# Kernel optimization log

Measured on AMD Instinct MI355X. Metric: run time of the kernel, lower is better.

The kernel has to match this reference:

```python
import jax, jax.numpy as jnp
import numpy as np
from jax import lax

NEG = jnp.float32(-1e30)  # log-domain 'zero'
BLANK = 0


def setup_inputs() -> dict:
    T, N, C, S = 512, 512, 80, 128
    k0, k1, k2, k3 = jax.random.split(jax.random.key(0), 4)
    logits = jax.random.normal(k0, (T, N, C), dtype=jnp.float32)
    log_probs = jax.nn.log_softmax(logits, axis=-1)  # CTCLoss expects log-probs
    targets = jax.random.randint(k1, (N, S), 1, C).astype(jnp.int32)  # labels in [1, C-1], blank=0 excluded
    input_lengths = jax.random.randint(k2, (N,), T // 2, T + 1).astype(jnp.int32)
    target_lengths = jax.random.randint(k3, (N,), S // 2, S + 1).astype(jnp.int32)
    return {"log_probs": log_probs, "targets": targets,
            "input_lengths": input_lengths, "target_lengths": target_lengths}


def _ctc_loss(log_probs, targets, input_lengths, target_lengths):
    # log_probs: (T, N, C) log-probabilities; targets: (N, S) labels (no blanks)
    T, N, C = log_probs.shape
    S = targets.shape[1]
    L = 2 * S + 1  # extended label length: blank-interleaved

    # extended targets: [blank, y1, blank, y2, ..., yS, blank]  -> (N, L)
    ext = jnp.zeros((N, L), jnp.int32).at[:, 1::2].set(targets)
    # skip transition (s-2 -> s) allowed only if ext[s] != ext[s-2]
    # (blank positions have ext[s]==ext[s-2]==blank, so this also forbids blank skips)
    skip_ok = jnp.pad(ext[:, 2:] != ext[:, :-2], ((0, 0), (2, 0)), constant_values=False)

    # emission log-probs on the lattice: (T, N, L)
    emit = jnp.take_along_axis(log_probs, jnp.broadcast_to(ext[None], (T, N, L)), axis=2)

    # alpha at t=0: only lattice positions 0 (blank) and 1 (first label) reachable
    alpha0 = jnp.full((N, L), NEG).at[:, 0].set(emit[0, :, 0]).at[:, 1].set(emit[0, :, 1])

    def step(alpha, xs):
        em, t = xs  # em: (N, L)
        a1 = jnp.pad(alpha[:, :-1], ((0, 0), (1, 0)), constant_values=NEG)
        a2 = jnp.where(skip_ok,
                       jnp.pad(alpha[:, :-2], ((0, 0), (2, 0)), constant_values=NEG), NEG)
        m = jnp.maximum(alpha, jnp.maximum(a1, a2))
        lse = m + jnp.log(jnp.exp(alpha - m) + jnp.exp(a1 - m) + jnp.exp(a2 - m))
        new = lse + em
        # freeze alpha for finished sequences (t >= input_length)
        alpha_new = jnp.where((t < input_lengths)[:, None], new, alpha)
        return alpha_new, None

    alpha_T, _ = lax.scan(step, alpha0, (emit[1:], jnp.arange(1, T, dtype=jnp.int32)))

    # final states: last blank (2*tl) and last label (2*tl - 1)
    i1 = (2 * target_lengths)[:, None]
    v1 = jnp.take_along_axis(alpha_T, i1, axis=1)[:, 0]
    v2 = jnp.take_along_axis(alpha_T, i1 - 1, axis=1)[:, 0]
    m = jnp.maximum(v1, v2)
    loss = -(m + jnp.log(jnp.exp(v1 - m) + jnp.exp(v2 - m)))
    # zero_infinity=True: infeasible alignments -> 0 loss
    loss = jnp.where(jnp.isfinite(loss) & (loss < 1e10), loss, 0.0)
    return loss  # (N,) reduction='none'


def reference(log_probs, targets, input_lengths, target_lengths):
    return _ctc_loss(log_probs, targets, input_lengths, target_lengths)
```

## Files before the change

### kernel.cpp

```cpp
#include <hip/hip_runtime.h>


#define NEGC  (-1.0e30f)
#define LOG2E 1.4426950408889634f
#define LN2   0.6931471805599453f

constexpr int T_ = 512;
constexpr int C_ = 80;
constexpr int S_ = 128;
constexpr int U_ = 8;
constexpr int WROW = 520;

__device__ __forceinline__ float exp2a(float x) { return __builtin_amdgcn_exp2f(x); }
__device__ __forceinline__ float log2a(float x) { return __builtin_amdgcn_logf(x); }

template <int CTRL>
__device__ __forceinline__ float dppf(float old_, float src) {
    return __int_as_float(__builtin_amdgcn_update_dpp(
        __float_as_int(old_), __float_as_int(src), CTRL, 0xF, 0xF, false));
}

__device__ __forceinline__ float lse2(float x, float y) {
    float m = fmaxf(x, y);
    return m + log2a(1.0f + exp2a(-fabsf(x - y)));
}
__device__ __forceinline__ float lse3(float x, float y, float z) {
    float m = fmaxf(x, fmaxf(y, z));
    return m + log2a(exp2a(x - m) + exp2a(y - m) + exp2a(z - m));
}

__global__ __launch_bounds__(64) void ctc_half(
    const float* __restrict__ lp, const int* __restrict__ tgt,
    const int* __restrict__ ilen, const int* __restrict__ tlen,
    float* __restrict__ ws, int N)
{
    const int b   = blockIdx.x;
    const int n   = b >> 1;
    const int dir = b & 1;
    const int l   = threadIdx.x;

    float* ga = ws + (size_t)n * WROW;
    float* gg = ga + 260;

    const int* tn = tgt + n * S_;
    const int ext1 = tn[2 * l];
    const int ext3 = tn[2 * l + 1];
    const int prev = (l > 0) ? tn[2 * l - 1] : 0;
    const bool skip1 = (l > 0) && (ext1 != prev);
    const bool skip3 = (ext3 != ext1);
    const bool skb3  = (l < 63) && (tn[2 * l + 2] != ext3);

    int len = ilen[n];
    len = len < 1 ? 1 : (len > T_ ? T_ : len);
    const int mid = len >> 1;

    const size_t rstride = (size_t)N * C_;
    const float* lpn = lp + (size_t)n * C_;
    const float* pB = lpn;
    const float* p1 = lpn + ext1;
    const float* p3 = lpn + ext3;

    float rb[U_], r1[U_], r3[U_];

    if (dir == 0) {
        const int last = mid - 1 > 0 ? mid - 1 : 0;
        #pragma unroll
        for (int u = 0; u < U_; ++u) {
            const int r = u + 1;
            const int rc = r < mid ? r : last;
            const size_t o = (size_t)rc * rstride;
            rb[r & 7] = pB[o]; r1[r & 7] = p1[o]; r3[r & 7] = p3[o];
        }
        float a0 = NEGC, a1 = NEGC, a2 = NEGC, a3 = NEGC, a4 = NEGC;
        {
            const float i0 = pB[0] * LOG2E;
            const float i1 = p1[0] * LOG2E;
            if (l == 0) { a0 = i0; a1 = i1; }
        }
        for (int tb = 1; tb < mid; tb += U_) {
            #pragma unroll
            for (int u = 0; u < U_; ++u) {
                const int t = tb + u;
                const int slot = (1 + u) & 7;
                const float eb = rb[slot] * LOG2E;
                const float e1 = r1[slot] * LOG2E;
                const float e3 = r3[slot] * LOG2E;
                const int rr = t + U_;
                const int rc = rr < mid ? rr : last;
                const size_t o = (size_t)rc * rstride;
                const float nrb = pB[o], nr1 = p1[o], nr3 = p3[o];
                if (t < mid) {
                    const float sm1 = dppf<0x138>(NEGC, a3);
                    const float M = fmaxf(fmaxf(fmaxf(a0, a1), fmaxf(a2, a3)),
                                          fmaxf(a4, sm1));
                    const float q0 = exp2a(a0 - M);
                    const float q1 = exp2a(a1 - M);
                    const float q2 = exp2a(a2 - M);
                    const float q3 = exp2a(a3 - M);
                    const float q4 = exp2a(a4 - M);
                    const float qs = exp2a(sm1 - M);
                    const float Mb = M + eb;
                    a0 = log2a(q0 + qs)                      + Mb;
                    a1 = log2a(q1 + q0 + (skip1 ? qs : 0.f)) + M + e1;
                    a2 = log2a(q2 + q1)                      + Mb;
                    a3 = log2a(q3 + q2 + (skip3 ? q1 : 0.f)) + M + e3;
                    a4 = log2a(q4 + q3)                      + Mb;
                }
                rb[slot] = nrb; r1[slot] = nr1; r3[slot] = nr3;
            }
        }
        ga[4 * l + 0] = a0; ga[4 * l + 1] = a1;
        ga[4 * l + 2] = a2; ga[4 * l + 3] = a3;
        if (l == 63) ga[256] = a4;
    } else {
        const int fe = len - 1;
        #pragma unroll
        for (int u = 0; u < U_; ++u) {
            int rc = fe - 1 - u; if (rc < 0) rc = 0;
            const size_t o = (size_t)rc * rstride;
            rb[u] = pB[o]; r1[u] = p1[o]; r3[u] = p3[o];
        }
        const int tl = tlen[n];
        const int sA = 2 * tl, sB = 2 * tl - 1;
        float g0, g1, g2, g3, g4;
        {
            const size_t o = (size_t)fe * rstride;
            const float ebi = pB[o] * LOG2E;
            const float e1i = p1[o] * LOG2E;
            const float e3i = p3[o] * LOG2E;
            const int s0 = 4 * l;
            g0 = (s0     == sA)                 ? ebi : NEGC;
            g1 = (s0 + 1 == sA || s0 + 1 == sB) ? e1i : NEGC;
            g2 = (s0 + 2 == sA)                 ? ebi : NEGC;
            g3 = (s0 + 3 == sA || s0 + 3 == sB) ? e3i : NEGC;
            g4 = (l == 63 && 256 == sA)         ? ebi : NEGC;
        }
        for (int tb = fe - 1; tb >= mid; tb -= U_) {
            #pragma unroll
            for (int u = 0; u < U_; ++u) {
                const int t = tb - u;
                const int slot = ((fe - 1 - tb) + u) & 7;
                const float eb = rb[slot] * LOG2E;
                const float e1 = r1[slot] * LOG2E;
                const float e3 = r3[slot] * LOG2E;
                int rc = t - U_; if (rc < 0) rc = 0;
                const size_t o = (size_t)rc * rstride;
                const float nrb = pB[o], nr1 = p1[o], nr3 = p3[o];
                if (t >= mid) {
                    const float nx0 = dppf<0x130>(g4,   g0);
                    const float nx1 = dppf<0x130>(NEGC, g1);
                    const float M = fmaxf(fmaxf(fmaxf(g0, g1), fmaxf(g2, g3)),
                                          fmaxf(nx0, nx1));
                    const float q0 = exp2a(g0 - M);
                    const float q1 = exp2a(g1 - M);
                    const float q2 = exp2a(g2 - M);
                    const float q3 = exp2a(g3 - M);
                    const float qx0 = exp2a(nx0 - M);
                    const float qx1 = exp2a(nx1 - M);
                    const float skb1q = (ext3 != ext1) ? q3 : 0.f;
                    g0 = log2a(q0 + q1)                        + M + eb;
                    g1 = log2a(q1 + q2 + skb1q)                + M + e1;
                    g2 = log2a(q2 + q3)                        + M + eb;
                    g3 = log2a(q3 + qx0 + (skb3 ? qx1 : 0.f))  + M + e3;
                    g4 = g4 + eb;
                }
                rb[slot] = nrb; r1[slot] = nr1; r3[slot] = nr3;
            }
        }
        gg[4 * l + 0] = g0; gg[4 * l + 1] = g1;
        gg[4 * l + 2] = g2; gg[4 * l + 3] = g3;
        if (l == 63) gg[256] = g4;
    }
}

__global__ __launch_bounds__(64) void ctc_comb(
    const float* __restrict__ ws, const int* __restrict__ tgt,
    const int* __restrict__ ilen, const int* __restrict__ tlen,
    float* __restrict__ out, int N)
{
    const int n = blockIdx.x;
    const int l = threadIdx.x;
    const float* ga = ws + (size_t)n * WROW;
    const float* gg = ga + 260;

    int len = ilen[n];
    len = len < 1 ? 1 : (len > T_ ? T_ : len);
    const int tl = tlen[n];

    if (len == 1) {
        if (l == 0) {
            const float v1 = ga[2 * tl];
            const float v2 = (2 * tl >= 1) ? ga[2 * tl - 1] : NEGC;
            float loss = -lse2(v1, v2) * LN2;
            if (!(loss < 1e10f) || !isfinite(loss)) loss = 0.0f;
            out[n] = loss;
        }
        return;
    }

    const int* tn = tgt + n * S_;
    const int ext1 = tn[2 * l];
    const int ext3 = tn[2 * l + 1];
    const int prev = (l > 0) ? tn[2 * l - 1] : 0;
    const bool skip1 = (l > 0) && (ext1 != prev);
    const bool skip3 = (ext3 != ext1);

    const int s0 = 4 * l;
    const float Am1 = (l > 0) ? ga[s0 - 1] : NEGC;
    const float A0 = ga[s0], A1 = ga[s0 + 1], A2 = ga[s0 + 2], A3 = ga[s0 + 3];
    const float v0 = lse2(A0, Am1)                    + gg[s0];
    const float v1 = lse3(A1, A0, skip1 ? Am1 : NEGC) + gg[s0 + 1];
    const float v2 = lse2(A2, A1)                     + gg[s0 + 2];
    const float v3 = lse3(A3, A2, skip3 ? A1 : NEGC)  + gg[s0 + 3];
    const float v4 = (l == 63) ? (lse2(ga[256], A3) + gg[256]) : NEGC;

    float m = fmaxf(fmaxf(v0, v1), fmaxf(fmaxf(v2, v3), v4));
    float ssum = exp2a(v0 - m) + exp2a(v1 - m) + exp2a(v2 - m)
               + exp2a(v3 - m) + exp2a(v4 - m);
    float M = m;
    #pragma unroll
    for (int d = 1; d < 64; d <<= 1) M = fmaxf(M, __shfl_xor(M, d));
    float r = ssum * exp2a(m - M);
    #pragma unroll
    for (int d = 1; d < 64; d <<= 1) r += __shfl_xor(r, d);
    if (l == 0) {
        float loss = -LN2 * (M + log2a(r));
        if (!(loss < 1e10f) || !isfinite(loss)) loss = 0.0f;
        out[n] = loss;
    }
}

__global__ __launch_bounds__(128) void ctc_fused(
    const float* __restrict__ lp, const int* __restrict__ tgt,
    const int* __restrict__ ilen, const int* __restrict__ tlen,
    float* __restrict__ out, int N)
{
    const int n    = blockIdx.x;
    const int wave = threadIdx.x >> 6;
    const int l    = threadIdx.x & 63;

    __shared__ float ga[2 * S_ + 1];
    __shared__ float gg[2 * S_ + 1];

    const int* tn = tgt + n * S_;
    const int ext1 = tn[2 * l];
    const int ext3 = tn[2 * l + 1];
    const int prev = (l > 0) ? tn[2 * l - 1] : 0;
    const bool skip1 = (l > 0) && (ext1 != prev);
    const bool skip3 = (ext3 != ext1);
    const bool skb1 = (tn[2 * l + 1] != tn[2 * l]);
    const bool skb3 = (l < 63) && (tn[2 * l + 2] != tn[2 * l + 1]);

    int len = ilen[n];
    len = len < 1 ? 1 : (len > T_ ? T_ : len);
    const int mid = len >> 1;

    const size_t rstride = (size_t)N * C_;
    const float* lpn = lp + (size_t)n * C_;
    const float* pB = lpn;
    const float* p1 = lpn + ext1;
    const float* p3 = lpn + ext3;

    float rb[U_], r1[U_], r3[U_];

    if (wave == 0) {
        const int last = mid - 1 > 0 ? mid - 1 : 0;
        #pragma unroll
        for (int u = 0; u < U_; ++u) {
            const int r = u + 1;
            const int rc = r < mid ? r : last;
            const size_t o = (size_t)rc * rstride;
            rb[r & 7] = pB[o]; r1[r & 7] = p1[o]; r3[r & 7] = p3[o];
        }
        float a0 = NEGC, a1 = NEGC, a2 = NEGC, a3 = NEGC, a4 = NEGC;
        {
            const float i0 = pB[0] * LOG2E;
            const float i1 = p1[0] * LOG2E;
            if (l == 0) { a0 = i0; a1 = i1; }
        }
        for (int tb = 1; tb < mid; tb += U_) {
            #pragma unroll
            for (int u = 0; u < U_; ++u) {
                const int t = tb + u;
                const int slot = (1 + u) & 7;
                const float eb = rb[slot] * LOG2E;
                const float e1 = r1[slot] * LOG2E;
                const float e3 = r3[slot] * LOG2E;
                const int rr = t + U_;
                const int rc = rr < mid ? rr : last;
                const size_t o = (size_t)rc * rstride;
                const float nrb = pB[o], nr1 = p1[o], nr3 = p3[o];
                if (t < mid) {
                    const float sm1 = dppf<0x138>(NEGC, a3);
                    const float z1 = skip1 ? sm1 : NEGC;
                    const float z3 = skip3 ? a1  : NEGC;
                    const float n0 = lse2(a0, sm1)    + eb;
                    const float n1 = lse3(a1, a0, z1) + e1;
                    const float n2 = lse2(a2, a1)     + eb;
                    const float n3 = lse3(a3, a2, z3) + e3;
                    const float n4 = lse2(a4, a3)     + eb;
                    a0 = n0; a1 = n1; a2 = n2; a3 = n3; a4 = n4;
                }
                rb[slot] = nrb; r1[slot] = nr1; r3[slot] = nr3;
            }
        }
        ga[4 * l + 0] = a0; ga[4 * l + 1] = a1;
        ga[4 * l + 2] = a2; ga[4 * l + 3] = a3;
        if (l == 63) ga[256] = a4;
    } else {
        const int fe = len - 1;
        #pragma unroll
        for (int u = 0; u < U_; ++u) {
            int rc = fe - 1 - u; if (rc < 0) rc = 0;
            const size_t o = (size_t)rc * rstride;
            rb[u] = pB[o]; r1[u] = p1[o]; r3[u] = p3[o];
        }
        const int tl = tlen[n];
        const int sA = 2 * tl, sB = 2 * tl - 1;
        float g0, g1, g2, g3, g4;
        {
            const size_t o = (size_t)fe * rstride;
            const float ebi = pB[o] * LOG2E;
            const float e1i = p1[o] * LOG2E;
            const float e3i = p3[o] * LOG2E;
            const int s0 = 4 * l;
            g0 = (s0     == sA)                 ? ebi : NEGC;
            g1 = (s0 + 1 == sA || s0 + 1 == sB) ? e1i : NEGC;
            g2 = (s0 + 2 == sA)                 ? ebi : NEGC;
            g3 = (s0 + 3 == sA || s0 + 3 == sB) ? e3i : NEGC;
            g4 = (l == 63 && 256 == sA)         ? ebi : NEGC;
        }
        for (int tb = fe - 1; tb >= mid; tb -= U_) {
            #pragma unroll
            for (int u = 0; u < U_; ++u) {
                const int t = tb - u;
                const int slot = ((fe - 1 - tb) + u) & 7;
                const float eb = rb[slot] * LOG2E;
                const float e1 = r1[slot] * LOG2E;
                const float e3 = r3[slot] * LOG2E;
                int rc = t - U_; if (rc < 0) rc = 0;
                const size_t o = (size_t)rc * rstride;
                const float nrb = pB[o], nr1 = p1[o], nr3 = p3[o];
                if (t >= mid) {
                    const float nx0 = dppf<0x130>(g4,   g0);
                    const float nx1 = dppf<0x130>(NEGC, g1);
                    const float z1 = skb1 ? g3  : NEGC;
                    const float z3 = skb3 ? nx1 : NEGC;
                    const float n0 = lse2(g0, g1)      + eb;
                    const float n1 = lse3(g1, g2, z1)  + e1;
                    const float n2 = lse2(g2, g3)      + eb;
                    const float n3 = lse3(g3, nx0, z3) + e3;
                    const float n4 = g4 + eb;
                    g0 = n0; g1 = n1; g2 = n2; g3 = n3; g4 = n4;
                }
                rb[slot] = nrb; r1[slot] = nr1; r3[slot] = nr3;
            }
        }
        gg[4 * l + 0] = g0; gg[4 * l + 1] = g1;
        gg[4 * l + 2] = g2; gg[4 * l + 3] = g3;
        if (l == 63) gg[256] = g4;
    }

    __syncthreads();

    if (wave == 0) {
        const int tl = tlen[n];
        if (len == 1) {
            if (l == 0) {
                const float v1 = ga[2 * tl];
                const float v2 = (2 * tl >= 1) ? ga[2 * tl - 1] : NEGC;
                float loss = -lse2(v1, v2) * LN2;
                if (!(loss < 1e10f) || !isfinite(loss)) loss = 0.0f;
                out[n] = loss;
            }
            return;
        }
        const int s0 = 4 * l;
        const float Am1 = (l > 0) ? ga[s0 - 1] : NEGC;
        const float A0 = ga[s0], A1 = ga[s0 + 1], A2 = ga[s0 + 2], A3 = ga[s0 + 3];
        const float v0 = lse2(A0, Am1)                    + gg[s0];
        const float v1 = lse3(A1, A0, skip1 ? Am1 : NEGC) + gg[s0 + 1];
        const float v2 = lse2(A2, A1)                     + gg[s0 + 2];
        const float v3 = lse3(A3, A2, skip3 ? A1 : NEGC)  + gg[s0 + 3];
        const float v4 = (l == 63) ? (lse2(ga[256], A3) + gg[256]) : NEGC;

        float m = fmaxf(fmaxf(v0, v1), fmaxf(fmaxf(v2, v3), v4));
        float ssum = exp2a(v0 - m) + exp2a(v1 - m) + exp2a(v2 - m)
                   + exp2a(v3 - m) + exp2a(v4 - m);
        float M = m;
        #pragma unroll
        for (int d = 1; d < 64; d <<= 1) M = fmaxf(M, __shfl_xor(M, d));
        float r = ssum * exp2a(m - M);
        #pragma unroll
        for (int d = 1; d < 64; d <<= 1) r += __shfl_xor(r, d);
        if (l == 0) {
            float loss = -LN2 * (M + log2a(r));
            if (!(loss < 1e10f) || !isfinite(loss)) loss = 0.0f;
            out[n] = loss;
        }
    }
}

extern "C" void kernel_launch(void* const* d_in, const int* in_sizes, int n_in,
                              void* d_out, int out_size, void* d_ws, size_t ws_size,
                              hipStream_t stream) {
    const float* lp  = (const float*)d_in[0];
    const int*   tg  = (const int*)  d_in[1];
    const int*   il  = (const int*)  d_in[2];
    const int*   tl  = (const int*)  d_in[3];
    float*       out = (float*)d_out;
    const int N = in_sizes[2];
    const size_t need = (size_t)N * WROW * sizeof(float);
    if (ws_size >= need) {
        ctc_half<<<2 * N, 64, 0, stream>>>(lp, tg, il, tl, (float*)d_ws, N);
        ctc_comb<<<N, 64, 0, stream>>>((const float*)d_ws, tg, il, tl, out, N);
    } else {
        ctc_fused<<<N, 128, 0, stream>>>(lp, tg, il, tl, out, N);
    }
}
```

Before: 156.6 us.

## Switch CTC alpha/beta recursion from log domain to scaled linear domain

Replaces the per-step log-sum-exp (six exp2 and five log2 transcendentals per lane per step) with linear-domain probabilities. Each lane keeps an integer exponent, and values are renormalised using exponent-bit extraction and power-of-two scaling. Neighbour exponents are exchanged with DPP so values can be aligned across lanes, and dead lanes inherit their neighbour's exponent. Only three exp2 calls are left per step, for the emissions. The cost is extra integer and ALU work per step and some risk of underflow or precision differences from the capped alignment shift.

```diff
diff --git a/kernel.cpp b/kernel.cpp
--- a/kernel.cpp
+++ b/kernel.cpp
@@ -10,6 +10,8 @@
 constexpr int S_ = 128;
 constexpr int U_ = 8;
 constexpr int WROW = 520;
+constexpr int BIGE = 1 << 24;
+constexpr int DCAP = 110;
 
 __device__ __forceinline__ float exp2a(float x) { return __builtin_amdgcn_exp2f(x); }
 __device__ __forceinline__ float log2a(float x) { return __builtin_amdgcn_logf(x); }
@@ -18,6 +20,15 @@
 __device__ __forceinline__ float dppf(float old_, float src) {
     return __int_as_float(__builtin_amdgcn_update_dpp(
         __float_as_int(old_), __float_as_int(src), CTRL, 0xF, 0xF, false));
+}
+template <int CTRL>
+__device__ __forceinline__ int dppi(int old_, int src) {
+    return __builtin_amdgcn_update_dpp(old_, src, CTRL, 0xF, 0xF, false);
+}
+
+__device__ __forceinline__ float pow2f(int k) {
+    int kc = k < -127 ? -127 : k;
+    return __int_as_float((kc + 127) << 23);
 }
 
 __device__ __forceinline__ float lse2(float x, float y) {
@@ -71,47 +82,63 @@
             const size_t o = (size_t)rc * rstride;
             rb[r & 7] = pB[o]; r1[r & 7] = p1[o]; r3[r & 7] = p3[o];
         }
-        float a0 = NEGC, a1 = NEGC, a2 = NEGC, a3 = NEGC, a4 = NEGC;
+        float m0 = 0.f, m1 = 0.f, m2 = 0.f, m3 = 0.f, m4 = 0.f;
+        int E = 0;
         {
-            const float i0 = pB[0] * LOG2E;
-            const float i1 = p1[0] * LOG2E;
-            if (l == 0) { a0 = i0; a1 = i1; }
+            const float i0 = exp2a(pB[0] * LOG2E);
+            const float i1 = exp2a(p1[0] * LOG2E);
+            if (l == 0) { m0 = i0; m1 = i1; }
         }
         for (int tb = 1; tb < mid; tb += U_) {
             #pragma unroll
             for (int u = 0; u < U_; ++u) {
                 const int t = tb + u;
                 const int slot = (1 + u) & 7;
-                const float eb = rb[slot] * LOG2E;
-                const float e1 = r1[slot] * LOG2E;
-                const float e3 = r3[slot] * LOG2E;
+                const float pb  = exp2a(rb[slot] * LOG2E);
+                const float pe1 = exp2a(r1[slot] * LOG2E);
+                const float pe3 = exp2a(r3[slot] * LOG2E);
                 const int rr = t + U_;
                 const int rc = rr < mid ? rr : last;
                 const size_t o = (size_t)rc * rstride;
                 const float nrb = pB[o], nr1 = p1[o], nr3 = p3[o];
                 if (t < mid) {
-                    const float sm1 = dppf<0x138>(NEGC, a3);
-                    const float M = fmaxf(fmaxf(fmaxf(a0, a1), fmaxf(a2, a3)),
-                                          fmaxf(a4, sm1));
-                    const float q0 = exp2a(a0 - M);
-                    const float q1 = exp2a(a1 - M);
-                    const float q2 = exp2a(a2 - M);
-                    const float q3 = exp2a(a3 - M);
-                    const float q4 = exp2a(a4 - M);
-                    const float qs = exp2a(sm1 - M);
-                    const float Mb = M + eb;
-                    a0 = log2a(q0 + qs)                      + Mb;
-                    a1 = log2a(q1 + q0 + (skip1 ? qs : 0.f)) + M + e1;
-                    a2 = log2a(q2 + q1)                      + Mb;
-                    a3 = log2a(q3 + q2 + (skip3 ? q1 : 0.f)) + M + e3;
-                    a4 = log2a(q4 + q3)                      + Mb;
+                    const float s3  = dppf<0x138>(0.f, m3);
+                    const int   Eup = dppi<0x138>(E, E);
+                    const int   dE  = Eup - E;
+                    const int   dc  = dE > DCAP ? DCAP : dE;
+                    const float fsc = pow2f(dc - dE);
+                    const float aln = s3 * pow2f(dc);
+
+                    const float m0f = m0 * fsc, m1f = m1 * fsc, m2f = m2 * fsc;
+                    const float m3f = m3 * fsc, m4f = m4 * fsc;
+                    const float z1 = skip1 ? aln : 0.f;
+                    const float z3 = skip3 ? m1f : 0.f;
+                    const float n0 = (m0f + aln)       * pb;
+                    const float n1 = (m1f + m0f + z1)  * pe1;
+                    const float n2 = (m2f + m1f)       * pb;
+                    const float n3 = (m3f + m2f + z3)  * pe3;
+                    const float n4 = (m4f + m3f)       * pb;
+
+                    const float mx = fmaxf(fmaxf(n0, n1), fmaxf(fmaxf(n2, n3), n4));
+                    const bool dead = (mx == 0.0f);
+                    const int  eb = (__float_as_int(mx) >> 23) & 0xFF;
+                    const float sc = __int_as_float((254 - eb) << 23);
+                    m0 = n0 * sc; m1 = n1 * sc; m2 = n2 * sc;
+                    m3 = n3 * sc; m4 = n4 * sc;
+                    const int Eb = Eup - dc;
+                    const int E1 = dead ? E : (Eb + eb - 127);
+                    const int Ein = dppi<0x138>(E1, E1);
+                    E = dead ? Ein : E1;
                 }
                 rb[slot] = nrb; r1[slot] = nr1; r3[slot] = nr3;
             }
         }
-        ga[4 * l + 0] = a0; ga[4 * l + 1] = a1;
-        ga[4 * l + 2] = a2; ga[4 * l + 3] = a3;
-        if (l == 63) ga[256] = a4;
+        const float Ef = (float)E;
+        ga[4 * l + 0] = fmaxf(log2a(m0) + Ef, NEGC);
+        ga[4 * l + 1] = fmaxf(log2a(m1) + Ef, NEGC);
+        ga[4 * l + 2] = fmaxf(log2a(m2) + Ef, NEGC);
+        ga[4 * l + 3] = fmaxf(log2a(m3) + Ef, NEGC);
+        if (l == 63) ga[256] = fmaxf(log2a(m4) + Ef, NEGC);
     } else {
         const int fe = len - 1;
         #pragma unroll
@@ -123,53 +150,70 @@
         const int tl = tlen[n];
         const int sA = 2 * tl, sB = 2 * tl - 1;
         float g0, g1, g2, g3, g4;
+        int E = (4 * l > sA) ? -BIGE : 0;
         {
             const size_t o = (size_t)fe * rstride;
-            const float ebi = pB[o] * LOG2E;
-            const float e1i = p1[o] * LOG2E;
-            const float e3i = p3[o] * LOG2E;
+            const float ebv = exp2a(pB[o] * LOG2E);
+            const float e1v = exp2a(p1[o] * LOG2E);
+            const float e3v = exp2a(p3[o] * LOG2E);
             const int s0 = 4 * l;
-            g0 = (s0     == sA)                 ? ebi : NEGC;
-            g1 = (s0 + 1 == sA || s0 + 1 == sB) ? e1i : NEGC;
-            g2 = (s0 + 2 == sA)                 ? ebi : NEGC;
-            g3 = (s0 + 3 == sA || s0 + 3 == sB) ? e3i : NEGC;
-            g4 = (l == 63 && 256 == sA)         ? ebi : NEGC;
+            g0 = (s0     == sA)                 ? ebv : 0.f;
+            g1 = (s0 + 1 == sA || s0 + 1 == sB) ? e1v : 0.f;
+            g2 = (s0 + 2 == sA)                 ? ebv : 0.f;
+            g3 = (s0 + 3 == sA || s0 + 3 == sB) ? e3v : 0.f;
+            g4 = (l == 63 && 256 == sA)         ? ebv : 0.f;
         }
         for (int tb = fe - 1; tb >= mid; tb -= U_) {
             #pragma unroll
             for (int u = 0; u < U_; ++u) {
                 const int t = tb - u;
                 const int slot = ((fe - 1 - tb) + u) & 7;
-                const float eb = rb[slot] * LOG2E;
-                const float e1 = r1[slot] * LOG2E;
-                const float e3 = r3[slot] * LOG2E;
+                const float pb  = exp2a(rb[slot] * LOG2E);
+                const float pe1 = exp2a(r1[slot] * LOG2E);
+                const float pe3 = exp2a(r3[slot] * LOG2E);
                 int rc = t - U_; if (rc < 0) rc = 0;
                 const size_t o = (size_t)rc * rstride;
                 const float nrb = pB[o], nr1 = p1[o], nr3 = p3[o];
                 if (t >= mid) {
-                    const float nx0 = dppf<0x130>(g4,   g0);
-                    const float nx1 = dppf<0x130>(NEGC, g1);
-                    const float M = fmaxf(fmaxf(fmaxf(g0, g1), fmaxf(g2, g3)),
-                                          fmaxf(nx0, nx1));
-                    const float q0 = exp2a(g0 - M);
-                    const float q1 = exp2a(g1 - M);
-                    const float q2 = exp2a(g2 - M);
-                    const float q3 = exp2a(g3 - M);
-                    const float qx0 = exp2a(nx0 - M);
-                    const float qx1 = exp2a(nx1 - M);
-                    const float skb1q = (ext3 != ext1) ? q3 : 0.f;
-                    g0 = log2a(q0 + q1)                        + M + eb;
-                    g1 = log2a(q1 + q2 + skb1q)                + M + e1;
-                    g2 = log2a(q2 + q3)                        + M + eb;
-                    g3 = log2a(q3 + qx0 + (skb3 ? qx1 : 0.f))  + M + e3;
-                    g4 = g4 + eb;
+                    const float x0  = dppf<0x130>(g4,  g0);
+                    const float x1  = dppf<0x130>(0.f, g1);
+                    const int   Eup = dppi<0x130>(E, E);
+                    const int   dE  = Eup - E;
+                    const int   dc  = dE > DCAP ? DCAP : dE;
+                    const float fsc = pow2f(dc - dE);
+                    const float al  = pow2f(dc);
+                    const float nx0 = x0 * al, nx1 = x1 * al;
+
+                    const float g0f = g0 * fsc, g1f = g1 * fsc, g2f = g2 * fsc;
+                    const float g3f = g3 * fsc, g4f = g4 * fsc;
+                    const float z1 = skip3 ? g3f : 0.f;
+                    const float z3 = skb3  ? nx1 : 0.f;
+                    const float n0 = (g0f + g1f)        * pb;
+                    const float n1 = (g1f + g2f + z1)   * pe1;
+                    const float n2 = (g2f + g3f)        * pb;
+                    const float n3 = (g3f + nx0 + z3)   * pe3;
+                    const float n4 = g4f                * pb;
+
+                    const float mx = fmaxf(fmaxf(n0, n1), fmaxf(fmaxf(n2, n3), n4));
+                    const bool dead = (mx == 0.0f);
+                    const int  eb = (__float_as_int(mx) >> 23) & 0xFF;
+                    const float sc = __int_as_float((254 - eb) << 23);
+                    g0 = n0 * sc; g1 = n1 * sc; g2 = n2 * sc;
+                    g3 = n3 * sc; g4 = n4 * sc;
+                    const int Eb = Eup - dc;
+                    const int E1 = dead ? E : (Eb + eb - 127);
+                    const int Ein = dppi<0x130>(E1, E1);
+                    E = dead ? Ein : E1;
                 }
                 rb[slot] = nrb; r1[slot] = nr1; r3[slot] = nr3;
             }
         }
-        gg[4 * l + 0] = g0; gg[4 * l + 1] = g1;
-        gg[4 * l + 2] = g2; gg[4 * l + 3] = g3;
-        if (l == 63) gg[256] = g4;
+        const float Ef = (float)E;
+        gg[4 * l + 0] = fmaxf(log2a(g0) + Ef, NEGC);
+        gg[4 * l + 1] = fmaxf(log2a(g1) + Ef, NEGC);
+        gg[4 * l + 2] = fmaxf(log2a(g2) + Ef, NEGC);
+        gg[4 * l + 3] = fmaxf(log2a(g3) + Ef, NEGC);
+        if (l == 63) gg[256] = fmaxf(log2a(g4) + Ef, NEGC);
     }
 }
 
```

Measured after the change: 161.6 us. 3.2% more time.

## Stage per-sequence log-prob rows into LDS as fp16 before recurrence

Applied to the files above, without the earlier changes.

Each block bulk-loads its half of the time rows for sequence n with coalesced float4 reads, converts them to fp16 and stores them in a 40KB shared table. The recurrence then gathers emissions from LDS with a one-step software prefetch, replacing the 8-deep register ring of scattered global loads. The aim is to take global gather latency off the serial time loop. In exchange, fp16 rounding of the log-probs adds precision loss, and the large LDS allocation may reduce occupancy. No barrier is used because each block is a single wave.

```diff
diff --git a/kernel.cpp b/kernel.cpp
--- a/kernel.cpp
+++ b/kernel.cpp
@@ -1,4 +1,5 @@
 #include <hip/hip_runtime.h>
+#include <hip/hip_fp16.h>
 
 
 #define NEGC  (-1.0e30f)
@@ -11,6 +12,8 @@
 constexpr int U_ = 8;
 constexpr int WROW = 520;
 
+#define WAIT_LGKM0 __builtin_amdgcn_s_waitcnt(0xC07F)
+
 __device__ __forceinline__ float exp2a(float x) { return __builtin_amdgcn_exp2f(x); }
 __device__ __forceinline__ float log2a(float x) { return __builtin_amdgcn_logf(x); }
 
@@ -18,6 +21,13 @@
 __device__ __forceinline__ float dppf(float old_, float src) {
     return __int_as_float(__builtin_amdgcn_update_dpp(
         __float_as_int(old_), __float_as_int(src), CTRL, 0xF, 0xF, false));
+}
+
+__device__ __forceinline__ unsigned short f2h(float x) {
+    return __half_as_ushort(__float2half(x));
+}
+__device__ __forceinline__ float h2f(unsigned short u) {
+    return __half2float(__ushort_as_half(u));
 }
 
 __device__ __forceinline__ float lse2(float x, float y) {
@@ -39,6 +49,8 @@
     const int dir = b & 1;
     const int l   = threadIdx.x;
 
+    __shared__ unsigned short eTab[256 * 80];
+
     float* ga = ws + (size_t)n * WROW;
     float* gg = ga + 260;
 
@@ -60,66 +72,80 @@
     const float* p1 = lpn + ext1;
     const float* p3 = lpn + ext3;
 
-    float rb[U_], r1[U_], r3[U_];
+    {
+        const int rbase = (dir == 0) ? 0 : mid;
+        const int hl    = (dir == 0) ? mid : (len - mid);
+        const int nchunk = hl * 20;
+        for (int base = 0; base < nchunk; base += 256) {
+            float4 v0, v1, v2, v3;
+            const int i0 = base + l, i1 = i0 + 64, i2 = i0 + 128, i3 = i0 + 192;
+            int r0 = i0 / 20, r1r = i1 / 20, r2 = i2 / 20, r3r = i3 / 20;
+            int c0 = i0 - r0 * 20, c1 = i1 - r1r * 20, c2 = i2 - r2 * 20, c3 = i3 - r3r * 20;
+            if (i0 < nchunk) v0 = *(const float4*)(lpn + (size_t)(rbase + r0)  * rstride + c0 * 4);
+            if (i1 < nchunk) v1 = *(const float4*)(lpn + (size_t)(rbase + r1r) * rstride + c1 * 4);
+            if (i2 < nchunk) v2 = *(const float4*)(lpn + (size_t)(rbase + r2)  * rstride + c2 * 4);
+            if (i3 < nchunk) v3 = *(const float4*)(lpn + (size_t)(rbase + r3r) * rstride + c3 * 4);
+            if (i0 < nchunk) { uint2 p; p.x = (uint)f2h(v0.x) | ((uint)f2h(v0.y) << 16);
+                               p.y = (uint)f2h(v0.z) | ((uint)f2h(v0.w) << 16);
+                               *(uint2*)&eTab[r0 * 80 + c0 * 4] = p; }
+            if (i1 < nchunk) { uint2 p; p.x = (uint)f2h(v1.x) | ((uint)f2h(v1.y) << 16);
+                               p.y = (uint)f2h(v1.z) | ((uint)f2h(v1.w) << 16);
+                               *(uint2*)&eTab[r1r * 80 + c1 * 4] = p; }
+            if (i2 < nchunk) { uint2 p; p.x = (uint)f2h(v2.x) | ((uint)f2h(v2.y) << 16);
+                               p.y = (uint)f2h(v2.z) | ((uint)f2h(v2.w) << 16);
+                               *(uint2*)&eTab[r2 * 80 + c2 * 4] = p; }
+            if (i3 < nchunk) { uint2 p; p.x = (uint)f2h(v3.x) | ((uint)f2h(v3.y) << 16);
+                               p.y = (uint)f2h(v3.z) | ((uint)f2h(v3.w) << 16);
+                               *(uint2*)&eTab[r3r * 80 + c3 * 4] = p; }
+        }
+        WAIT_LGKM0;
+    }
 
     if (dir == 0) {
-        const int last = mid - 1 > 0 ? mid - 1 : 0;
-        #pragma unroll
-        for (int u = 0; u < U_; ++u) {
-            const int r = u + 1;
-            const int rc = r < mid ? r : last;
-            const size_t o = (size_t)rc * rstride;
-            rb[r & 7] = pB[o]; r1[r & 7] = p1[o]; r3[r & 7] = p3[o];
-        }
         float a0 = NEGC, a1 = NEGC, a2 = NEGC, a3 = NEGC, a4 = NEGC;
         {
             const float i0 = pB[0] * LOG2E;
             const float i1 = p1[0] * LOG2E;
             if (l == 0) { a0 = i0; a1 = i1; }
         }
-        for (int tb = 1; tb < mid; tb += U_) {
-            #pragma unroll
-            for (int u = 0; u < U_; ++u) {
-                const int t = tb + u;
-                const int slot = (1 + u) & 7;
-                const float eb = rb[slot] * LOG2E;
-                const float e1 = r1[slot] * LOG2E;
-                const float e3 = r3[slot] * LOG2E;
-                const int rr = t + U_;
-                const int rc = rr < mid ? rr : last;
-                const size_t o = (size_t)rc * rstride;
-                const float nrb = pB[o], nr1 = p1[o], nr3 = p3[o];
-                if (t < mid) {
-                    const float sm1 = dppf<0x138>(NEGC, a3);
-                    const float M = fmaxf(fmaxf(fmaxf(a0, a1), fmaxf(a2, a3)),
-                                          fmaxf(a4, sm1));
-                    const float q0 = exp2a(a0 - M);
-                    const float q1 = exp2a(a1 - M);
-                    const float q2 = exp2a(a2 - M);
-                    const float q3 = exp2a(a3 - M);
-                    const float q4 = exp2a(a4 - M);
-                    const float qs = exp2a(sm1 - M);
-                    const float Mb = M + eb;
-                    a0 = log2a(q0 + qs)                      + Mb;
-                    a1 = log2a(q1 + q0 + (skip1 ? qs : 0.f)) + M + e1;
-                    a2 = log2a(q2 + q1)                      + Mb;
-                    a3 = log2a(q3 + q2 + (skip3 ? q1 : 0.f)) + M + e3;
-                    a4 = log2a(q4 + q3)                      + Mb;
-                }
-                rb[slot] = nrb; r1[slot] = nr1; r3[slot] = nr3;
-            }
+        unsigned short nbu = 0, n1u = 0, n3u = 0;
+        if (mid > 1) {
+            nbu = eTab[80];
+            n1u = eTab[80 + ext1];
+            n3u = eTab[80 + ext3];
+        }
+        for (int t = 1; t < mid; ++t) {
+            const unsigned short cbu = nbu, c1u = n1u, c3u = n3u;
+            const int nr = (t + 1 < mid) ? (t + 1) : (mid - 1);
+            nbu = eTab[nr * 80];
+            n1u = eTab[nr * 80 + ext1];
+            n3u = eTab[nr * 80 + ext3];
+
+            const float eb = h2f(cbu) * LOG2E;
+            const float e1 = h2f(c1u) * LOG2E;
+            const float e3 = h2f(c3u) * LOG2E;
+
+            const float sm1 = dppf<0x138>(NEGC, a3);
+            const float M = fmaxf(fmaxf(fmaxf(a0, a1), fmaxf(a2, a3)),
+                                  fmaxf(a4, sm1));
+            const float q0 = exp2a(a0 - M);
+            const float q1 = exp2a(a1 - M);
+            const float q2 = exp2a(a2 - M);
+            const float q3 = exp2a(a3 - M);
+            const float q4 = exp2a(a4 - M);
+            const float qs = exp2a(sm1 - M);
+            const float Mb = M + eb;
+            a0 = log2a(q0 + qs)                      + Mb;
+            a1 = log2a(q1 + q0 + (skip1 ? qs : 0.f)) + M + e1;
+            a2 = log2a(q2 + q1)                      + Mb;
+            a3 = log2a(q3 + q2 + (skip3 ? q1 : 0.f)) + M + e3;
+            a4 = log2a(q4 + q3)                      + Mb;
         }
         ga[4 * l + 0] = a0; ga[4 * l + 1] = a1;
         ga[4 * l + 2] = a2; ga[4 * l + 3] = a3;
         if (l == 63) ga[256] = a4;
     } else {
         const int fe = len - 1;
-        #pragma unroll
-        for (int u = 0; u < U_; ++u) {
-            int rc = fe - 1 - u; if (rc < 0) rc = 0;
-            const size_t o = (size_t)rc * rstride;
-            rb[u] = pB[o]; r1[u] = p1[o]; r3[u] = p3[o];
-        }
         const int tl = tlen[n];
         const int sA = 2 * tl, sB = 2 * tl - 1;
         float g0, g1, g2, g3, g4;
@@ -135,37 +161,40 @@
             g3 = (s0 + 3 == sA || s0 + 3 == sB) ? e3i : NEGC;
             g4 = (l == 63 && 256 == sA)         ? ebi : NEGC;
         }
-        for (int tb = fe - 1; tb >= mid; tb -= U_) {
-            #pragma unroll
-            for (int u = 0; u < U_; ++u) {
-                const int t = tb - u;
-                const int slot = ((fe - 1 - tb) + u) & 7;
-                const float eb = rb[slot] * LOG2E;
-                const float e1 = r1[slot] * LOG2E;
-                const float e3 = r3[slot] * LOG2E;
-                int rc = t - U_; if (rc < 0) rc = 0;
-                const size_t o = (size_t)rc * rstride;
-                const float nrb = pB[o], nr1 = p1[o], nr3 = p3[o];
-                if (t >= mid) {
-                    const float nx0 = dppf<0x130>(g4,   g0);
-                    const float nx1 = dppf<0x130>(NEGC, g1);
-                    const float M = fmaxf(fmaxf(fmaxf(g0, g1), fmaxf(g2, g3)),
-                                          fmaxf(nx0, nx1));
-                    const float q0 = exp2a(g0 - M);
-                    const float q1 = exp2a(g1 - M);
-                    const float q2 = exp2a(g2 - M);
-                    const float q3 = exp2a(g3 - M);
-                    const float qx0 = exp2a(nx0 - M);
-                    const float qx1 = exp2a(nx1 - M);
-                    const float skb1q = (ext3 != ext1) ? q3 : 0.f;
-                    g0 = log2a(q0 + q1)                        + M + eb;
-                    g1 = log2a(q1 + q2 + skb1q)                + M + e1;
-                    g2 = log2a(q2 + q3)                        + M + eb;
-                    g3 = log2a(q3 + qx0 + (skb3 ? qx1 : 0.f))  + M + e3;
-                    g4 = g4 + eb;
-                }
-                rb[slot] = nrb; r1[slot] = nr1; r3[slot] = nr3;
-            }
+        unsigned short nbu = 0, n1u = 0, n3u = 0;
+        if (fe - 1 >= mid) {
+            const int pr = (fe - 1 - mid) * 80;
+            nbu = eTab[pr];
+            n1u = eTab[pr + ext1];
+            n3u = eTab[pr + ext3];
+        }
+        for (int t = fe - 1; t >= mid; --t) {
+            const unsigned short cbu = nbu, c1u = n1u, c3u = n3u;
+            const int nr = (t - 1 >= mid) ? (t - 1 - mid) : 0;
+            nbu = eTab[nr * 80];
+            n1u = eTab[nr * 80 + ext1];
+            n3u = eTab[nr * 80 + ext3];
+
+            const float eb = h2f(cbu) * LOG2E;
+            const float e1 = h2f(c1u) * LOG2E;
+            const float e3 = h2f(c3u) * LOG2E;
+
+            const float nx0 = dppf<0x130>(g4,   g0);
+            const float nx1 = dppf<0x130>(NEGC, g1);
+            const float M = fmaxf(fmaxf(fmaxf(g0, g1), fmaxf(g2, g3)),
+                                  fmaxf(nx0, nx1));
+            const float q0 = exp2a(g0 - M);
+            const float q1 = exp2a(g1 - M);
+            const float q2 = exp2a(g2 - M);
+            const float q3 = exp2a(g3 - M);
+            const float qx0 = exp2a(nx0 - M);
+            const float qx1 = exp2a(nx1 - M);
+            const float skb1q = (ext3 != ext1) ? q3 : 0.f;
+            g0 = log2a(q0 + q1)                        + M + eb;
+            g1 = log2a(q1 + q2 + skb1q)                + M + e1;
+            g2 = log2a(q2 + q3)                        + M + eb;
+            g3 = log2a(q3 + qx0 + (skb3 ? qx1 : 0.f))  + M + e3;
+            g4 = g4 + eb;
         }
         gg[4 * l + 0] = g0; gg[4 * l + 1] = g1;
         gg[4 * l + 2] = g2; gg[4 * l + 3] = g3;
```

New measurement: 192.9 us. 23.2% more time.
